# Kernel optimization log

Measured on AMD Instinct MI355X. Metric: run time of the kernel, lower is better.

The kernel has to match this reference:

```python
import jax, jax.numpy as jnp
import numpy as np

B, N, D, H = 16, 1024, 384, 6
DH = D // H  # 64 per-head dim


def _layernorm(x, w, b, eps=1e-5):
    mu = jnp.mean(x, axis=-1, keepdims=True)
    var = jnp.var(x, axis=-1, keepdims=True)
    return (x - mu) * jax.lax.rsqrt(var + eps) * w + b


def setup_inputs() -> dict:
    key = jax.random.key(0)
    ks = jax.random.split(key, 10)
    std = 0.02
    return {
        "X": jax.random.normal(ks[0], (B, N, D), dtype=jnp.float32),
        "Wq": jax.random.normal(ks[1], (H, DH, D), dtype=jnp.float32) * std,
        "Wk": jax.random.normal(ks[2], (H, DH, D), dtype=jnp.float32) * std,
        "Wv": jax.random.normal(ks[3], (H, DH, D), dtype=jnp.float32) * std,
        "Wo": jax.random.normal(ks[4], (D, D), dtype=jnp.float32) * std,
        "bo": jnp.zeros((D,), dtype=jnp.float32),
        "ln1_w": jnp.ones((D,), dtype=jnp.float32),
        "ln1_b": jnp.zeros((D,), dtype=jnp.float32),
        "ln2_w": jnp.ones((D,), dtype=jnp.float32),
        "ln2_b": jnp.zeros((D,), dtype=jnp.float32),
        "W1": jax.random.normal(ks[5], (2 * D, D), dtype=jnp.float32) * std,
        "b1": jnp.zeros((2 * D,), dtype=jnp.float32),
        "W2": jax.random.normal(ks[6], (D, 2 * D), dtype=jnp.float32) * std,
        "b2": jnp.zeros((D,), dtype=jnp.float32),
    }


def reference(X, Wq, Wk, Wv, Wo, bo, ln1_w, ln1_b, ln2_w, ln2_b, W1, b1, W2, b2):
    scale = 1.0 / jnp.sqrt(jnp.float32(DH))
    # pre-LN then multi-head attention (heads vectorized, math identical to per-head loop)
    t = _layernorm(X, ln1_w, ln1_b)                       # [B,N,D]
    q = jnp.einsum('bnd,hkd->bhnk', t, Wq)                # [B,H,N,DH]
    k = jnp.einsum('bnd,hkd->bhnk', t, Wk)
    v = jnp.einsum('bnd,hkd->bhnk', t, Wv)
    scores = jnp.einsum('bhnk,bhmk->bhnm', q, k) * scale  # [B,H,N,N]
    p = jax.nn.softmax(scores, axis=-1)
    o = jnp.einsum('bhnm,bhmk->bhnk', p, v)               # [B,H,N,DH]
    o = jnp.transpose(o, (0, 2, 1, 3)).reshape(B, N, D)   # concat heads
    attn = o @ Wo.T + bo
    # residual + post-LN (dropout/drop_path are identity in eval)
    X2 = _layernorm(X + attn, ln2_w, ln2_b)
    # MLP: Linear -> exact GELU -> Linear
    h = jax.nn.gelu(X2 @ W1.T + b1, approximate=False)
    mlp = h @ W2.T + b2
    return X2 + mlp
```

## Files before the change

kernel.cpp:

```cpp
#include <hip/hip_runtime.h>
#include <math.h>

typedef float  f32x4  __attribute__((ext_vector_type(4)));
typedef __bf16 bf16x8 __attribute__((ext_vector_type(8)));
typedef __bf16 bf16x4 __attribute__((ext_vector_type(4)));

__device__ __forceinline__ void gload16(const void* g, void* l) {
  __builtin_amdgcn_global_load_lds((__attribute__((address_space(1))) const void*)g,
                                   (__attribute__((address_space(3))) void*)l, 16, 0, 0);
}

__device__ __forceinline__ f32x4 mfma16(bf16x8 a, bf16x8 b, f32x4 c) {
  return __builtin_amdgcn_mfma_f32_16x16x32_bf16(a, b, c, 0, 0, 0);
}

__device__ __forceinline__ float fast_gelu(float x) {
  const float xs = x * 0.70710678118654752f;
  const float ax = fabsf(xs);
  const float t  = __builtin_amdgcn_rcpf(1.f + 0.3275911f * ax);
  const float poly = ((((1.061405429f*t - 1.453152027f)*t + 1.421413741f)*t
                       - 0.284496736f)*t + 0.254829592f)*t;
  const float e = __builtin_amdgcn_exp2f(-1.4426950408889634f * ax * ax);
  float erfv = 1.f - poly * e;
  erfv = (xs < 0.f) ? -erfv : erfv;
  return 0.5f * x * (1.f + erfv);
}

__global__ __launch_bounds__(256) void prep_kernel(
    const float* __restrict__ X, const float* __restrict__ ln1w, const float* __restrict__ ln1b,
    __bf16* __restrict__ t_bf,
    const float* __restrict__ Wq, const float* __restrict__ Wk, const float* __restrict__ Wv,
    const float* __restrict__ Wo, const float* __restrict__ W1, const float* __restrict__ W2,
    __bf16* __restrict__ wqkv, __bf16* __restrict__ wo, __bf16* __restrict__ w1, __bf16* __restrict__ w2)
{
  if (blockIdx.x >= 4096) {
    const int idx = ((blockIdx.x - 4096) * 256 + threadIdx.x) * 4;
    const float* src; __bf16* dst; int off;
    if      (idx < 147456) { src = Wq; dst = wqkv;          off = idx; }
    else if (idx < 294912) { src = Wk; dst = wqkv + 147456; off = idx - 147456; }
    else if (idx < 442368) { src = Wv; dst = wqkv + 294912; off = idx - 294912; }
    else if (idx < 589824) { src = Wo; dst = wo;            off = idx - 442368; }
    else if (idx < 884736) { src = W1; dst = w1;            off = idx - 589824; }
    else                   { src = W2; dst = w2;            off = idx - 884736; }
    f32x4 v = *(const f32x4*)(src + off);
    bf16x4 o = {(__bf16)v.x, (__bf16)v.y, (__bf16)v.z, (__bf16)v.w};
    *(bf16x4*)(dst + off) = o;
    return;
  }
  const int row  = blockIdx.x * 4 + (threadIdx.x >> 6);
  const int lane = threadIdx.x & 63;
  const float* x = X + (size_t)row * 384;
  float v[6]; float s = 0.f;
#pragma unroll
  for (int j = 0; j < 6; ++j) { v[j] = x[lane + 64*j]; s += v[j]; }
#pragma unroll
  for (int off = 32; off > 0; off >>= 1) s += __shfl_xor(s, off);
  const float mu = s * (1.f/384.f);
  float s2 = 0.f;
#pragma unroll
  for (int j = 0; j < 6; ++j) { float d = v[j] - mu; s2 += d*d; }
#pragma unroll
  for (int off = 32; off > 0; off >>= 1) s2 += __shfl_xor(s2, off);
  const float inv = rsqrtf(s2 * (1.f/384.f) + 1e-5f);
#pragma unroll
  for (int j = 0; j < 6; ++j) {
    const int cidx = lane + 64*j;
    t_bf[(size_t)row*384 + cidx] = (__bf16)((v[j]-mu)*inv*ln1w[cidx] + ln1b[cidx]);
  }
}

__global__ __launch_bounds__(256) void ln_kernel(
    const float* __restrict__ in, const float* __restrict__ w, const float* __restrict__ b,
    __bf16* __restrict__ outb, float* __restrict__ outf)
{
  const int row  = blockIdx.x * 4 + (threadIdx.x >> 6);
  const int lane = threadIdx.x & 63;
  const float* x = in + (size_t)row * 384;
  float v[6]; float s = 0.f;
#pragma unroll
  for (int j = 0; j < 6; ++j) { v[j] = x[lane + 64*j]; s += v[j]; }
#pragma unroll
  for (int off = 32; off > 0; off >>= 1) s += __shfl_xor(s, off);
  const float mu = s * (1.f/384.f);
  float s2 = 0.f;
#pragma unroll
  for (int j = 0; j < 6; ++j) { float d = v[j] - mu; s2 += d*d; }
#pragma unroll
  for (int off = 32; off > 0; off >>= 1) s2 += __shfl_xor(s2, off);
  const float inv = rsqrtf(s2 * (1.f/384.f) + 1e-5f);
#pragma unroll
  for (int j = 0; j < 6; ++j) {
    const int cidx = lane + 64*j;
    const float y = (v[j]-mu)*inv*w[cidx] + b[cidx];
    outb[(size_t)row*384 + cidx] = (__bf16)y;
    outf[(size_t)row*384 + cidx] = y;
  }
}

template<int EPI>
__global__ __launch_bounds__(256, 3) void gemm_bt(
    const __bf16* __restrict__ A, const __bf16* __restrict__ Bw,
    int N, int K,
    const float* __restrict__ bias, const float* __restrict__ resid,
    float* __restrict__ outf, __bf16* __restrict__ outb,
    __bf16* __restrict__ q_out, __bf16* __restrict__ k_out, __bf16* __restrict__ vt_out)
{
  __shared__ __attribute__((aligned(16))) __bf16 As[2][4096];
  __shared__ __attribute__((aligned(16))) __bf16 Bs[2][4096];
  const int tid  = threadIdx.x;
  const int lane = tid & 63;
  const int w    = tid >> 6;
  const int wm   = w >> 1, wn = w & 1;
  const int m0   = blockIdx.x * 128, n0 = blockIdx.y * 128;

  f32x4 acc[4][4] = {};

  const int srow = lane & 15, skq = lane >> 4;
  const __bf16* gptr[4];
  __bf16*       lptr[4];
#pragma unroll
  for (int r = 0; r < 4; ++r) {
    const int id = r * 4 + w;
    if (id < 8) {
      gptr[r] = A + (size_t)(m0 + id*16 + srow) * K + (skq << 3);
      lptr[r] = &As[0][id * 512];
    } else {
      const int j = id - 8;
      gptr[r] = Bw + (size_t)(n0 + j*16 + srow) * K + (skq << 3);
      lptr[r] = &Bs[0][j * 512];
    }
  }

  auto stage = [&](int kk, int b) {
#pragma unroll
    for (int r = 0; r < 4; ++r)
      gload16(gptr[r] + kk * 32, lptr[r] + b * 4096);
  };
  auto compute = [&](int b) {
    bf16x8 af[4], bfr[4];
#pragma unroll
    for (int i = 0; i < 4; ++i)
      af[i] = *(const bf16x8*)&As[b][(wm*4 + i) * 512 + lane * 8];
#pragma unroll
    for (int j = 0; j < 4; ++j)
      bfr[j] = *(const bf16x8*)&Bs[b][(wn*4 + j) * 512 + lane * 8];
#pragma unroll
    for (int i = 0; i < 4; ++i)
#pragma unroll
      for (int j = 0; j < 4; ++j)
        acc[i][j] = mfma16(af[i], bfr[j], acc[i][j]);
  };

  const int NIT = K >> 5;
  stage(0, 0);
  __syncthreads();
  for (int k = 0; k < NIT; ++k) {
    const int b = k & 1;
    if (k + 1 < NIT) stage(k + 1, b ^ 1);
    compute(b);
    __syncthreads();
  }

  const int quad = lane >> 4, cc = lane & 15;
#pragma unroll
  for (int rt = 0; rt < 4; ++rt) {
#pragma unroll
    for (int ct = 0; ct < 4; ++ct) {
      const int gr0 = m0 + (wm*4 + rt)*16 + quad*4;
      const int gc  = n0 + (wn*4 + ct)*16 + cc;
      f32x4 a = acc[rt][ct];
      if constexpr (EPI == 0) {
        const int bb = gr0 >> 10, nn = gr0 & 1023;
        if (gc >= 768) {
          const int jj = gc - 768, hh = jj >> 6, dh = jj & 63;
          bf16x4 pk = {(__bf16)a[0], (__bf16)a[1], (__bf16)a[2], (__bf16)a[3]};
          *(bf16x4*)&vt_out[((size_t)((bb*6 + hh)*64 + dh) << 10) + nn] = pk;
        } else {
          const bool isq = (gc < 384);
          const int jj = isq ? gc : (gc - 384);
          __bf16* dst = isq ? q_out : k_out;
          const float sc = isq ? 0.18033688011112042f : 1.0f;
          const int hh = jj >> 6, dh = jj & 63;
#pragma unroll
          for (int i = 0; i < 4; ++i)
            dst[((size_t)(((bb*6 + hh) << 10) | (nn + i)) << 6) + dh] = (__bf16)(a[i] * sc);
        }
      } else {
#pragma unroll
        for (int i = 0; i < 4; ++i) {
          const int gr = gr0 + i;
          float val = a[i];
          if constexpr (EPI == 1) {
            const size_t idx = (size_t)gr * N + gc;
            outf[idx] = val + bias[gc] + resid[idx];
          } else if constexpr (EPI == 2) {
            outb[(size_t)gr * N + gc] = (__bf16)fast_gelu(val + bias[gc]);
          } else {
            const size_t idx = (size_t)gr * N + gc;
            outf[idx] = outf[idx] + val + bias[gc];
          }
        }
      }
    }
  }
}

__global__ __launch_bounds__(256, 3) void attn_kernel(
    const __bf16* __restrict__ qp, const __bf16* __restrict__ kp,
    const __bf16* __restrict__ vtp, __bf16* __restrict__ omat)
{
  __shared__ __attribute__((aligned(16))) __bf16 Ks[2][4096];
  __shared__ __attribute__((aligned(16))) __bf16 Vs[2][4096];
  __shared__ __attribute__((aligned(16))) __bf16 Ps[4][2][1088];
  const int tid = threadIdx.x, lane = tid & 63, w = tid >> 6;
  const int bh = blockIdx.x;
  const int q0 = blockIdx.y * 128 + w * 32;
  const int quad = lane >> 4, lo = lane & 15;

  bf16x8 qa[2][2];
#pragma unroll
  for (int t = 0; t < 2; ++t) {
    const __bf16* qb = qp + ((size_t)bh * 1024 + q0 + t*16 + lo) * 64 + (quad << 3);
    qa[t][0] = *(const bf16x8*)qb;
    qa[t][1] = *(const bf16x8*)(qb + 32);
  }

  f32x4 oacc[2][4] = {};
  float l_r[2] = {0.f, 0.f};

  auto stage = [&](int c, int bb) {
#pragma unroll
    for (int s = 0; s < 2; ++s) {
      const int ck = s * 256 + tid;
      const int l = ck & 63, g = ck >> 6;
      const int ct = g >> 1, ks = g & 1;
      const __bf16* gk = kp + ((size_t)bh*1024 + c*64 + ct*16 + (l & 15)) * 64
                            + ks*32 + ((l >> 4) << 3);
      gload16(gk, &Ks[bb][(ck & ~63) * 8]);
      const __bf16* gv = vtp + (((size_t)(bh*64 + ct*16 + (l & 15))) << 10)
                             + c*64 + ks*32 + ((l >> 4) << 3);
      gload16(gv, &Vs[bb][(ck & ~63) * 8]);
    }
  };

  stage(0, 0);
  __syncthreads();

  for (int c = 0; c < 16; ++c) {
    const int bb = c & 1;
    if (c + 1 < 16) stage(c + 1, bb ^ 1);

    f32x4 st[2][4];
#pragma unroll
    for (int ct = 0; ct < 4; ++ct) {
      bf16x8 kb0 = *(const bf16x8*)&Ks[bb][((ct*2 + 0)*64 + lane) * 8];
      bf16x8 kb1 = *(const bf16x8*)&Ks[bb][((ct*2 + 1)*64 + lane) * 8];
#pragma unroll
      for (int t = 0; t < 2; ++t) {
        f32x4 s0 = {};
        s0 = mfma16(kb0, qa[t][0], s0);
        s0 = mfma16(kb1, qa[t][1], s0);
        st[t][ct] = s0;
      }
    }
#pragma unroll
    for (int t = 0; t < 2; ++t)
#pragma unroll
      for (int ct = 0; ct < 4; ++ct) {
        const float p0 = __builtin_amdgcn_exp2f(st[t][ct][0]);
        const float p1 = __builtin_amdgcn_exp2f(st[t][ct][1]);
        const float p2 = __builtin_amdgcn_exp2f(st[t][ct][2]);
        const float p3 = __builtin_amdgcn_exp2f(st[t][ct][3]);
        l_r[t] += (p0 + p1) + (p2 + p3);
        bf16x4 pk = {(__bf16)p0, (__bf16)p1, (__bf16)p2, (__bf16)p3};
        *(bf16x4*)&Ps[w][t][lo*68 + ct*16 + quad*4] = pk;
      }
    bf16x8 pa[2][2];
#pragma unroll
    for (int t = 0; t < 2; ++t)
#pragma unroll
      for (int ks = 0; ks < 2; ++ks)
        pa[t][ks] = *(const bf16x8*)&Ps[w][t][lo*68 + ks*32 + (quad << 3)];
#pragma unroll
    for (int dt = 0; dt < 4; ++dt)
#pragma unroll
      for (int ks = 0; ks < 2; ++ks) {
        bf16x8 vb = *(const bf16x8*)&Vs[bb][((dt*2 + ks)*64 + lane) * 8];
#pragma unroll
        for (int t = 0; t < 2; ++t)
          oacc[t][dt] = mfma16(pa[t][ks], vb, oacc[t][dt]);
      }
    __syncthreads();
  }

  const int b = bh / 6, h = bh - (bh / 6) * 6;
#pragma unroll
  for (int t = 0; t < 2; ++t) {
    float ls = l_r[t];
    ls += __shfl_xor(ls, 16);
    ls += __shfl_xor(ls, 32);
#pragma unroll
    for (int i = 0; i < 4; ++i) {
      const float linv = 1.f / __shfl(ls, quad*4 + i);
      const int n = q0 + t*16 + quad*4 + i;
#pragma unroll
      for (int dt = 0; dt < 4; ++dt)
        omat[((size_t)((b << 10) | n)) * 384 + (h << 6) + dt*16 + lo] =
            (__bf16)(oacc[t][dt][i] * linv);
    }
  }
}

extern "C" void kernel_launch(void* const* d_in, const int* in_sizes, int n_in,
                              void* d_out, int out_size, void* d_ws, size_t ws_size,
                              hipStream_t stream)
{
  const float* X    = (const float*)d_in[0];
  const float* Wq   = (const float*)d_in[1];
  const float* Wk   = (const float*)d_in[2];
  const float* Wv   = (const float*)d_in[3];
  const float* Wo   = (const float*)d_in[4];
  const float* bo   = (const float*)d_in[5];
  const float* ln1w = (const float*)d_in[6];
  const float* ln1b = (const float*)d_in[7];
  const float* ln2w = (const float*)d_in[8];
  const float* ln2b = (const float*)d_in[9];
  const float* W1   = (const float*)d_in[10];
  const float* b1   = (const float*)d_in[11];
  const float* W2   = (const float*)d_in[12];
  const float* b2   = (const float*)d_in[13];

  char* ws = (char*)d_ws;
  __bf16* t_bf  = (__bf16*)(ws + 0);
  __bf16* q_bf  = (__bf16*)(ws + 12582912);
  __bf16* k_bf  = (__bf16*)(ws + 25165824);
  __bf16* omat  = (__bf16*)(ws + 37748736);
  __bf16* vt_bf = (__bf16*)(ws + 50331648);
  float*  s1    = (float*) (ws + 62914560);
  __bf16* h_bf  = (__bf16*)(ws + 62914560);
  __bf16* wqkv  = (__bf16*)(ws + 88080384);
  __bf16* wo_b  = (__bf16*)(ws + 88965120);
  __bf16* w1_b  = (__bf16*)(ws + 89260032);
  __bf16* w2_b  = (__bf16*)(ws + 89849856);
  __bf16* x2_bf = t_bf;
  float*  out   = (float*)d_out;

  prep_kernel<<<5248, 256, 0, stream>>>(X, ln1w, ln1b, t_bf,
      Wq, Wk, Wv, Wo, W1, W2, wqkv, wo_b, w1_b, w2_b);
  gemm_bt<0><<<dim3(128,9), 256, 0, stream>>>(t_bf, wqkv, 1152, 384,
      nullptr, nullptr, nullptr, nullptr, q_bf, k_bf, vt_bf);
  attn_kernel<<<dim3(96,8), 256, 0, stream>>>(q_bf, k_bf, vt_bf, omat);
  gemm_bt<1><<<dim3(128,3), 256, 0, stream>>>(omat, wo_b, 384, 384,
      bo, X, s1, nullptr, nullptr, nullptr, nullptr);
  ln_kernel<<<4096, 256, 0, stream>>>(s1, ln2w, ln2b, x2_bf, out);
  gemm_bt<2><<<dim3(128,6), 256, 0, stream>>>(x2_bf, w1_b, 768, 384,
      b1, nullptr, nullptr, h_bf, nullptr, nullptr, nullptr);
  gemm_bt<3><<<dim3(128,3), 256, 0, stream>>>(h_bf, w2_b, 384, 768,
      b2, nullptr, out, nullptr, nullptr, nullptr, nullptr);
}
```

Before: 270.9 us.

## Use FP8 MFMA for output projection and MLP GEMMs

Converts Wo, W1 and W2 to FP8 in the prep kernel. The attention output, the LN2 output and the GELU activations are now written as FP8, and the out-projection and both MLP GEMMs run through a new FP8 16x16x32 MFMA kernel with a 64-wide K tile. This halves operand bytes and intermediate traffic for those GEMMs and uses the higher-throughput FP8 matrix path. The cost is a large precision loss on activations and weights, which may exceed the output tolerance.

```diff
diff --git a/kernel.cpp b/kernel.cpp
--- a/kernel.cpp
+++ b/kernel.cpp
@@ -12,6 +12,14 @@
 
 __device__ __forceinline__ f32x4 mfma16(bf16x8 a, bf16x8 b, f32x4 c) {
   return __builtin_amdgcn_mfma_f32_16x16x32_bf16(a, b, c, 0, 0, 0);
+}
+
+__device__ __forceinline__ f32x4 mfma8(long a, long b, f32x4 c) {
+  return __builtin_amdgcn_mfma_f32_16x16x32_fp8_fp8(a, b, c, 0, 0, 0);
+}
+
+__device__ __forceinline__ unsigned char f2fp8(float x) {
+  return (unsigned char)__builtin_amdgcn_cvt_pk_fp8_f32(x, x, 0, false);
 }
 
 __device__ __forceinline__ float fast_gelu(float x) {
@@ -31,20 +39,29 @@
     __bf16* __restrict__ t_bf,
     const float* __restrict__ Wq, const float* __restrict__ Wk, const float* __restrict__ Wv,
     const float* __restrict__ Wo, const float* __restrict__ W1, const float* __restrict__ W2,
-    __bf16* __restrict__ wqkv, __bf16* __restrict__ wo, __bf16* __restrict__ w1, __bf16* __restrict__ w2)
+    __bf16* __restrict__ wqkv, unsigned char* __restrict__ wo8,
+    unsigned char* __restrict__ w18, unsigned char* __restrict__ w28)
 {
   if (blockIdx.x >= 4096) {
     const int idx = ((blockIdx.x - 4096) * 256 + threadIdx.x) * 4;
-    const float* src; __bf16* dst; int off;
-    if      (idx < 147456) { src = Wq; dst = wqkv;          off = idx; }
-    else if (idx < 294912) { src = Wk; dst = wqkv + 147456; off = idx - 147456; }
-    else if (idx < 442368) { src = Wv; dst = wqkv + 294912; off = idx - 294912; }
-    else if (idx < 589824) { src = Wo; dst = wo;            off = idx - 442368; }
-    else if (idx < 884736) { src = W1; dst = w1;            off = idx - 589824; }
-    else                   { src = W2; dst = w2;            off = idx - 884736; }
-    f32x4 v = *(const f32x4*)(src + off);
-    bf16x4 o = {(__bf16)v.x, (__bf16)v.y, (__bf16)v.z, (__bf16)v.w};
-    *(bf16x4*)(dst + off) = o;
+    if (idx < 442368) {
+      const float* src; __bf16* dst; int off;
+      if      (idx < 147456) { src = Wq; dst = wqkv;          off = idx; }
+      else if (idx < 294912) { src = Wk; dst = wqkv + 147456; off = idx - 147456; }
+      else                   { src = Wv; dst = wqkv + 294912; off = idx - 294912; }
+      f32x4 v = *(const f32x4*)(src + off);
+      bf16x4 o = {(__bf16)v.x, (__bf16)v.y, (__bf16)v.z, (__bf16)v.w};
+      *(bf16x4*)(dst + off) = o;
+    } else {
+      const float* src; unsigned char* dst; int off;
+      if      (idx < 589824) { src = Wo; dst = wo8; off = idx - 442368; }
+      else if (idx < 884736) { src = W1; dst = w18; off = idx - 589824; }
+      else                   { src = W2; dst = w28; off = idx - 884736; }
+      f32x4 v = *(const f32x4*)(src + off);
+      int p = __builtin_amdgcn_cvt_pk_fp8_f32(v.x, v.y, 0, false);
+      p     = __builtin_amdgcn_cvt_pk_fp8_f32(v.z, v.w, p, true);
+      *(int*)(dst + off) = p;
+    }
     return;
   }
   const int row  = blockIdx.x * 4 + (threadIdx.x >> 6);
@@ -71,7 +88,7 @@
 
 __global__ __launch_bounds__(256) void ln_kernel(
     const float* __restrict__ in, const float* __restrict__ w, const float* __restrict__ b,
-    __bf16* __restrict__ outb, float* __restrict__ outf)
+    unsigned char* __restrict__ outc, float* __restrict__ outf)
 {
   const int row  = blockIdx.x * 4 + (threadIdx.x >> 6);
   const int lane = threadIdx.x & 63;
@@ -92,17 +109,13 @@
   for (int j = 0; j < 6; ++j) {
     const int cidx = lane + 64*j;
     const float y = (v[j]-mu)*inv*w[cidx] + b[cidx];
-    outb[(size_t)row*384 + cidx] = (__bf16)y;
+    outc[(size_t)row*384 + cidx] = f2fp8(y);
     outf[(size_t)row*384 + cidx] = y;
   }
 }
 
-template<int EPI>
-__global__ __launch_bounds__(256, 3) void gemm_bt(
-    const __bf16* __restrict__ A, const __bf16* __restrict__ Bw,
-    int N, int K,
-    const float* __restrict__ bias, const float* __restrict__ resid,
-    float* __restrict__ outf, __bf16* __restrict__ outb,
+__global__ __launch_bounds__(256, 3) void gemm_qkv(
+    const __bf16* __restrict__ A, const __bf16* __restrict__ Bw, int K,
     __bf16* __restrict__ q_out, __bf16* __restrict__ k_out, __bf16* __restrict__ vt_out)
 {
   __shared__ __attribute__((aligned(16))) __bf16 As[2][4096];
@@ -121,14 +134,9 @@
 #pragma unroll
   for (int r = 0; r < 4; ++r) {
     const int id = r * 4 + w;
-    if (id < 8) {
-      gptr[r] = A + (size_t)(m0 + id*16 + srow) * K + (skq << 3);
-      lptr[r] = &As[0][id * 512];
-    } else {
-      const int j = id - 8;
-      gptr[r] = Bw + (size_t)(n0 + j*16 + srow) * K + (skq << 3);
-      lptr[r] = &Bs[0][j * 512];
-    }
+    if (id < 8) { gptr[r] = A  + (size_t)(m0 + id*16 + srow) * K + (skq << 3); lptr[r] = &As[0][id * 512]; }
+    else        { const int j = id - 8;
+                  gptr[r] = Bw + (size_t)(n0 + j*16 + srow) * K + (skq << 3); lptr[r] = &Bs[0][j * 512]; }
   }
 
   auto stage = [&](int kk, int b) {
@@ -139,11 +147,9 @@
   auto compute = [&](int b) {
     bf16x8 af[4], bfr[4];
 #pragma unroll
-    for (int i = 0; i < 4; ++i)
-      af[i] = *(const bf16x8*)&As[b][(wm*4 + i) * 512 + lane * 8];
-#pragma unroll
-    for (int j = 0; j < 4; ++j)
-      bfr[j] = *(const bf16x8*)&Bs[b][(wn*4 + j) * 512 + lane * 8];
+    for (int i = 0; i < 4; ++i) af[i]  = *(const bf16x8*)&As[b][(wm*4 + i) * 512 + lane * 8];
+#pragma unroll
+    for (int j = 0; j < 4; ++j) bfr[j] = *(const bf16x8*)&Bs[b][(wn*4 + j) * 512 + lane * 8];
 #pragma unroll
     for (int i = 0; i < 4; ++i)
 #pragma unroll
@@ -169,36 +175,106 @@
       const int gr0 = m0 + (wm*4 + rt)*16 + quad*4;
       const int gc  = n0 + (wn*4 + ct)*16 + cc;
       f32x4 a = acc[rt][ct];
-      if constexpr (EPI == 0) {
-        const int bb = gr0 >> 10, nn = gr0 & 1023;
-        if (gc >= 768) {
-          const int jj = gc - 768, hh = jj >> 6, dh = jj & 63;
-          bf16x4 pk = {(__bf16)a[0], (__bf16)a[1], (__bf16)a[2], (__bf16)a[3]};
-          *(bf16x4*)&vt_out[((size_t)((bb*6 + hh)*64 + dh) << 10) + nn] = pk;
+      const int bb = gr0 >> 10, nn = gr0 & 1023;
+      if (gc >= 768) {
+        const int jj = gc - 768, hh = jj >> 6, dh = jj & 63;
+        bf16x4 pk = {(__bf16)a[0], (__bf16)a[1], (__bf16)a[2], (__bf16)a[3]};
+        *(bf16x4*)&vt_out[((size_t)((bb*6 + hh)*64 + dh) << 10) + nn] = pk;
+      } else {
+        const bool isq = (gc < 384);
+        const int jj = isq ? gc : (gc - 384);
+        __bf16* dst = isq ? q_out : k_out;
+        const float sc = isq ? 0.18033688011112042f : 1.0f;
+        const int hh = jj >> 6, dh = jj & 63;
+#pragma unroll
+        for (int i = 0; i < 4; ++i)
+          dst[((size_t)(((bb*6 + hh) << 10) | (nn + i)) << 6) + dh] = (__bf16)(a[i] * sc);
+      }
+    }
+  }
+}
+
+template<int EPI>
+__global__ __launch_bounds__(256, 3) void gemm_f8(
+    const unsigned char* __restrict__ A, const unsigned char* __restrict__ Bw,
+    int N, int K,
+    const float* __restrict__ bias, const float* __restrict__ resid,
+    float* __restrict__ outf, unsigned char* __restrict__ outc)
+{
+  __shared__ __attribute__((aligned(16))) unsigned char As[2][8192];
+  __shared__ __attribute__((aligned(16))) unsigned char Bs[2][8192];
+  const int tid  = threadIdx.x;
+  const int lane = tid & 63;
+  const int w    = tid >> 6;
+  const int wm   = w >> 1, wn = w & 1;
+  const int m0   = blockIdx.x * 128, n0 = blockIdx.y * 128;
+
+  f32x4 acc[4][4] = {};
+
+  const int srow = lane >> 2, skq = (lane & 3) << 4;
+  const unsigned char* gptr[4];
+  unsigned char*       lptr[4];
+#pragma unroll
+  for (int r = 0; r < 4; ++r) {
+    const int id = r * 4 + w;
+    if (id < 8) { gptr[r] = A  + (size_t)(m0 + id*16 + srow) * K + skq; lptr[r] = &As[0][id * 1024]; }
+    else        { const int j = id - 8;
+                  gptr[r] = Bw + (size_t)(n0 + j*16 + srow) * K + skq; lptr[r] = &Bs[0][j * 1024]; }
+  }
+
+  auto stage = [&](int kk, int b) {
+#pragma unroll
+    for (int r = 0; r < 4; ++r)
+      gload16(gptr[r] + kk * 64, lptr[r] + b * 8192);
+  };
+  const int lo = lane & 15, quad = lane >> 4;
+  auto compute = [&](int b) {
+#pragma unroll
+    for (int s = 0; s < 2; ++s) {
+      long af[4], bfr[4];
+#pragma unroll
+      for (int i = 0; i < 4; ++i)
+        af[i]  = *(const long*)&As[b][(wm*4 + i) * 1024 + lo*64 + s*32 + quad*8];
+#pragma unroll
+      for (int j = 0; j < 4; ++j)
+        bfr[j] = *(const long*)&Bs[b][(wn*4 + j) * 1024 + lo*64 + s*32 + quad*8];
+#pragma unroll
+      for (int i = 0; i < 4; ++i)
+#pragma unroll
+        for (int j = 0; j < 4; ++j)
+          acc[i][j] = mfma8(af[i], bfr[j], acc[i][j]);
+    }
+  };
+
+  const int NIT = K >> 6;
+  stage(0, 0);
+  __syncthreads();
+  for (int k = 0; k < NIT; ++k) {
+    const int b = k & 1;
+    if (k + 1 < NIT) stage(k + 1, b ^ 1);
+    compute(b);
+    __syncthreads();
+  }
+
+#pragma unroll
+  for (int rt = 0; rt < 4; ++rt) {
+#pragma unroll
+    for (int ct = 0; ct < 4; ++ct) {
+      const int gr0 = m0 + (wm*4 + rt)*16 + quad*4;
+      const int gc  = n0 + (wn*4 + ct)*16 + lo;
+      f32x4 a = acc[rt][ct];
+#pragma unroll
+      for (int i = 0; i < 4; ++i) {
+        const int gr = gr0 + i;
+        float val = a[i];
+        if constexpr (EPI == 1) {
+          const size_t idx = (size_t)gr * N + gc;
+          outf[idx] = val + bias[gc] + resid[idx];
+        } else if constexpr (EPI == 2) {
+          outc[(size_t)gr * N + gc] = f2fp8(fast_gelu(val + bias[gc]));
         } else {
-          const bool isq = (gc < 384);
-          const int jj = isq ? gc : (gc - 384);
-          __bf16* dst = isq ? q_out : k_out;
-          const float sc = isq ? 0.18033688011112042f : 1.0f;
-          const int hh = jj >> 6, dh = jj & 63;
-#pragma unroll
-          for (int i = 0; i < 4; ++i)
-            dst[((size_t)(((bb*6 + hh) << 10) | (nn + i)) << 6) + dh] = (__bf16)(a[i] * sc);
-        }
-      } else {
-#pragma unroll
-        for (int i = 0; i < 4; ++i) {
-          const int gr = gr0 + i;
-          float val = a[i];
-          if constexpr (EPI == 1) {
-            const size_t idx = (size_t)gr * N + gc;
-            outf[idx] = val + bias[gc] + resid[idx];
-          } else if constexpr (EPI == 2) {
-            outb[(size_t)gr * N + gc] = (__bf16)fast_gelu(val + bias[gc]);
-          } else {
-            const size_t idx = (size_t)gr * N + gc;
-            outf[idx] = outf[idx] + val + bias[gc];
-          }
+          const size_t idx = (size_t)gr * N + gc;
+          outf[idx] = outf[idx] + val + bias[gc];
         }
       }
     }
@@ -207,7 +283,7 @@
 
 __global__ __launch_bounds__(256, 3) void attn_kernel(
     const __bf16* __restrict__ qp, const __bf16* __restrict__ kp,
-    const __bf16* __restrict__ vtp, __bf16* __restrict__ omat)
+    const __bf16* __restrict__ vtp, unsigned char* __restrict__ omat8)
 {
   __shared__ __attribute__((aligned(16))) __bf16 Ks[2][4096];
   __shared__ __attribute__((aligned(16))) __bf16 Vs[2][4096];
@@ -305,8 +381,8 @@
       const int n = q0 + t*16 + quad*4 + i;
 #pragma unroll
       for (int dt = 0; dt < 4; ++dt)
-        omat[((size_t)((b << 10) | n)) * 384 + (h << 6) + dt*16 + lo] =
-            (__bf16)(oacc[t][dt][i] * linv);
+        omat8[((size_t)((b << 10) | n)) * 384 + (h << 6) + dt*16 + lo] =
+            f2fp8(oacc[t][dt][i] * linv);
     }
   }
 }
@@ -332,29 +408,28 @@
 
   char* ws = (char*)d_ws;
   __bf16* t_bf  = (__bf16*)(ws + 0);
+  unsigned char* x2_f8 = (unsigned char*)(ws + 0);
   __bf16* q_bf  = (__bf16*)(ws + 12582912);
   __bf16* k_bf  = (__bf16*)(ws + 25165824);
-  __bf16* omat  = (__bf16*)(ws + 37748736);
+  unsigned char* omat8 = (unsigned char*)(ws + 37748736);
   __bf16* vt_bf = (__bf16*)(ws + 50331648);
   float*  s1    = (float*) (ws + 62914560);
-  __bf16* h_bf  = (__bf16*)(ws + 62914560);
+  unsigned char* h8 = (unsigned char*)(ws + 62914560);
   __bf16* wqkv  = (__bf16*)(ws + 88080384);
-  __bf16* wo_b  = (__bf16*)(ws + 88965120);
-  __bf16* w1_b  = (__bf16*)(ws + 89260032);
-  __bf16* w2_b  = (__bf16*)(ws + 89849856);
-  __bf16* x2_bf = t_bf;
+  unsigned char* wo8 = (unsigned char*)(ws + 88965120);
+  unsigned char* w18 = (unsigned char*)(ws + 89112576);
+  unsigned char* w28 = (unsigned char*)(ws + 89407488);
   float*  out   = (float*)d_out;
 
   prep_kernel<<<5248, 256, 0, stream>>>(X, ln1w, ln1b, t_bf,
-      Wq, Wk, Wv, Wo, W1, W2, wqkv, wo_b, w1_b, w2_b);
-  gemm_bt<0><<<dim3(128,9), 256, 0, stream>>>(t_bf, wqkv, 1152, 384,
-      nullptr, nullptr, nullptr, nullptr, q_bf, k_bf, vt_bf);
-  attn_kernel<<<dim3(96,8), 256, 0, stream>>>(q_bf, k_bf, vt_bf, omat);
-  gemm_bt<1><<<dim3(128,3), 256, 0, stream>>>(omat, wo_b, 384, 384,
-      bo, X, s1, nullptr, nullptr, nullptr, nullptr);
-  ln_kernel<<<4096, 256, 0, stream>>>(s1, ln2w, ln2b, x2_bf, out);
-  gemm_bt<2><<<dim3(128,6), 256, 0, stream>>>(x2_bf, w1_b, 768, 384,
-      b1, nullptr, nullptr, h_bf, nullptr, nullptr, nullptr);
-  gemm_bt<3><<<dim3(128,3), 256, 0, stream>>>(h_bf, w2_b, 384, 768,
-      b2, nullptr, out, nullptr, nullptr, nullptr, nullptr);
-}
+      Wq, Wk, Wv, Wo, W1, W2, wqkv, wo8, w18, w28);
+  gemm_qkv<<<dim3(128,9), 256, 0, stream>>>(t_bf, wqkv, 384, q_bf, k_bf, vt_bf);
+  attn_kernel<<<dim3(96,8), 256, 0, stream>>>(q_bf, k_bf, vt_bf, omat8);
+  gemm_f8<1><<<dim3(128,3), 256, 0, stream>>>(omat8, wo8, 384, 384,
+      bo, X, s1, nullptr);
+  ln_kernel<<<4096, 256, 0, stream>>>(s1, ln2w, ln2b, x2_f8, out);
+  gemm_f8<2><<<dim3(128,6), 256, 0, stream>>>(x2_f8, w18, 768, 384,
+      b1, nullptr, nullptr, h8);
+  gemm_f8<3><<<dim3(128,3), 256, 0, stream>>>(h8, w28, 384, 768,
+      b2, nullptr, out, nullptr);
+}
```

Result: no change. 274.6 us (+1.4%).
